# Optimization experiments

Hardware: AMD Instinct MI355X
Metric: run time of the kernel (lower is better)

The kernel has to match this reference:

```python
import jax, jax.numpy as jnp
import numpy as np

B, T, C, H = 2, 2048, 1024, 16
HD = C // H  # 64

def setup_inputs() -> dict:
    key = jax.random.key(0)
    ks = jax.random.split(key, 9)
    s = 0.02
    return {
        "x": jax.random.normal(ks[0], (B, T, C), jnp.float32),
        "Wq": jax.random.normal(ks[1], (C, C), jnp.float32) * s,
        "bq": jax.random.normal(ks[2], (C,), jnp.float32) * s,
        "Wk": jax.random.normal(ks[3], (C, C), jnp.float32) * s,
        "bk": jax.random.normal(ks[4], (C,), jnp.float32) * s,
        "Wv": jax.random.normal(ks[5], (C, C), jnp.float32) * s,
        "bv": jax.random.normal(ks[6], (C,), jnp.float32) * s,
        "Wp": jax.random.normal(ks[7], (C, C), jnp.float32) * s,
        "bp": jax.random.normal(ks[8], (C,), jnp.float32) * s,
    }

def reference(x, Wq, bq, Wk, bk, Wv, bv, Wp, bp):
    Bb, Tt, Cc = x.shape
    hd = Cc // H
    # project and split heads: [B, H, T, hd]
    def heads(W, b):
        return (x @ W.T + b).reshape(Bb, Tt, H, hd).transpose(0, 2, 1, 3)
    q, k, v = heads(Wq, bq), heads(Wk, bk), heads(Wv, bv)
    scale = 1.0 / np.sqrt(hd).astype(np.float32)
    att = jnp.einsum('bhqd,bhkd->bhqk', q, k) * scale
    causal = jnp.tril(jnp.ones((Tt, Tt), bool))
    att = jnp.where(causal[None, None], att, -jnp.inf)
    att = jax.nn.softmax(att, axis=-1)
    y = jnp.einsum('bhqk,bhkd->bhqd', att, v)
    y = y.transpose(0, 2, 1, 3).reshape(Bb, Tt, Cc)
    return y @ Wp.T + bp
```

## Files before the change

### kernel.cpp

```cpp
#include <hip/hip_runtime.h>
#include <hip/hip_bf16.h>

#define Tsz 2048
#define Csz 1024
#define Hn 16

typedef short s8v __attribute__((ext_vector_type(8)));
typedef short s4v __attribute__((ext_vector_type(4)));
typedef float f4v __attribute__((ext_vector_type(4)));

#define QSCALE (0.125f * 1.44269504088896f)

__device__ __forceinline__ short bf_bits(float x) {
    __hip_bfloat16 t = __float2bfloat16(x);
    return *reinterpret_cast<short*>(&t);
}

__device__ __forceinline__ void gload_lds(const void* g, void* l) {
    __builtin_amdgcn_global_load_lds(
        (const __attribute__((address_space(1))) void*)g,
        (__attribute__((address_space(3))) void*)l, 16, 0, 0);
}

__global__ void cvt5(const float* __restrict__ x, const float* __restrict__ wq,
                     const float* __restrict__ wk, const float* __restrict__ wv,
                     const float* __restrict__ wp,
                     short* __restrict__ xo, short* __restrict__ qo,
                     short* __restrict__ ko, short* __restrict__ vo,
                     short* __restrict__ po) {
    const int y = blockIdx.y;
    const float* in; short* out; int n;
    switch (y) {
        case 0: in = x;  out = xo; n = 2 * Tsz * Csz; break;
        case 1: in = wq; out = qo; n = Csz * Csz; break;
        case 2: in = wk; out = ko; n = Csz * Csz; break;
        case 3: in = wv; out = vo; n = Csz * Csz; break;
        default: in = wp; out = po; n = Csz * Csz; break;
    }
    int i = (blockIdx.x * blockDim.x + threadIdx.x) * 4;
    if (i >= n) return;
    float4 v = *(const float4*)(in + i);
    short4 o;
    o.x = bf_bits(v.x); o.y = bf_bits(v.y); o.z = bf_bits(v.z); o.w = bf_bits(v.w);
    *(short4*)(out + i) = o;
}

__global__ __launch_bounds__(256, 2) void qkv_gemm(
    const short* __restrict__ X,
    const short* __restrict__ Wq, const short* __restrict__ Wk, const short* __restrict__ Wv,
    const float* __restrict__ bq, const float* __restrict__ bk, const float* __restrict__ bv,
    short* __restrict__ Qo, short* __restrict__ Ko, short* __restrict__ Vto)
{
    const int z = blockIdx.z;
    const short* W = (z == 0) ? Wq : (z == 1) ? Wk : Wv;
    const float* bias = (z == 0) ? bq : (z == 1) ? bk : bv;

    __shared__ __align__(16) short Ash[128 * 32];
    __shared__ __align__(16) short Bsh[128 * 32];

    const int tid = threadIdx.x, lane = tid & 63, wave = tid >> 6;
    const int ln = lane & 15, hi = lane >> 4;
    const int m0 = blockIdx.x * 128, n0 = blockIdx.y * 128;
    const int wm = (wave >> 1) * 64, wn = (wave & 1) * 64;

    const short* Ag = X + (size_t)(m0 + (tid >> 2)) * Csz + (tid & 3) * 8;
    const short* Bg = W + (size_t)(n0 + (tid >> 2)) * Csz + (tid & 3) * 8;

    f4v acc[4][4];
    #pragma unroll
    for (int mt = 0; mt < 4; mt++)
        #pragma unroll
        for (int nt = 0; nt < 4; nt++)
            #pragma unroll
            for (int i = 0; i < 4; i++) acc[mt][nt][i] = 0.f;

    for (int k0 = 0; k0 < Csz; k0 += 32) {
        __syncthreads();
        gload_lds(Ag + k0, Ash + tid * 8);
        gload_lds(Ag + k0 + (size_t)64 * Csz, Ash + 2048 + tid * 8);
        gload_lds(Bg + k0, Bsh + tid * 8);
        gload_lds(Bg + k0 + (size_t)64 * Csz, Bsh + 2048 + tid * 8);
        __syncthreads();

        s8v af[4], bfr[4];
        #pragma unroll
        for (int mt = 0; mt < 4; mt++)
            af[mt] = *(const s8v*)(Ash + (wm + mt * 16 + ln) * 32 + hi * 8);
        #pragma unroll
        for (int nt = 0; nt < 4; nt++)
            bfr[nt] = *(const s8v*)(Bsh + (wn + nt * 16 + ln) * 32 + hi * 8);
        #pragma unroll
        for (int mt = 0; mt < 4; mt++)
            #pragma unroll
            for (int nt = 0; nt < 4; nt++)
                acc[mt][nt] = __builtin_amdgcn_mfma_f32_16x16x32_bf16(af[mt], bfr[nt], acc[mt][nt], 0, 0, 0);
    }

    const float scale = (z == 0) ? QSCALE : 1.0f;
    short* out = (z == 0) ? Qo : Ko;

    #pragma unroll
    for (int nt = 0; nt < 4; nt++) {
        const int col = n0 + wn + nt * 16 + ln;
        const float bvv = bias[col];
        #pragma unroll
        for (int mt = 0; mt < 4; mt++) {
            const int row0 = m0 + wm + mt * 16 + hi * 4;
            if (z == 2) {
                const int b = row0 >> 11, t = row0 & 2047;
                s4v pk;
                #pragma unroll
                for (int i = 0; i < 4; i++) pk[i] = bf_bits(acc[mt][nt][i] + bvv);
                *(s4v*)(Vto + (size_t)(b * 1024 + col) * Tsz + t) = pk;
            } else {
                #pragma unroll
                for (int i = 0; i < 4; i++)
                    out[(size_t)(row0 + i) * Csz + col] = bf_bits((acc[mt][nt][i] + bvv) * scale);
            }
        }
    }
}

__global__ __launch_bounds__(256, 2) void proj_gemm(
    const short* __restrict__ A, const short* __restrict__ W,
    const float* __restrict__ bias, float* __restrict__ out)
{
    __shared__ __align__(16) short Ash[128 * 32];
    __shared__ __align__(16) short Bsh[128 * 32];

    const int tid = threadIdx.x, lane = tid & 63, wave = tid >> 6;
    const int ln = lane & 15, hi = lane >> 4;
    const int m0 = blockIdx.x * 128, n0 = blockIdx.y * 128;
    const int wm = (wave >> 1) * 64, wn = (wave & 1) * 64;

    const short* Ag = A + (size_t)(m0 + (tid >> 2)) * Csz + (tid & 3) * 8;
    const short* Bg = W + (size_t)(n0 + (tid >> 2)) * Csz + (tid & 3) * 8;

    f4v acc[4][4];
    #pragma unroll
    for (int mt = 0; mt < 4; mt++)
        #pragma unroll
        for (int nt = 0; nt < 4; nt++)
            #pragma unroll
            for (int i = 0; i < 4; i++) acc[mt][nt][i] = 0.f;

    for (int k0 = 0; k0 < Csz; k0 += 32) {
        __syncthreads();
        gload_lds(Ag + k0, Ash + tid * 8);
        gload_lds(Ag + k0 + (size_t)64 * Csz, Ash + 2048 + tid * 8);
        gload_lds(Bg + k0, Bsh + tid * 8);
        gload_lds(Bg + k0 + (size_t)64 * Csz, Bsh + 2048 + tid * 8);
        __syncthreads();

        s8v af[4], bfr[4];
        #pragma unroll
        for (int mt = 0; mt < 4; mt++)
            af[mt] = *(const s8v*)(Ash + (wm + mt * 16 + ln) * 32 + hi * 8);
        #pragma unroll
        for (int nt = 0; nt < 4; nt++)
            bfr[nt] = *(const s8v*)(Bsh + (wn + nt * 16 + ln) * 32 + hi * 8);
        #pragma unroll
        for (int mt = 0; mt < 4; mt++)
            #pragma unroll
            for (int nt = 0; nt < 4; nt++)
                acc[mt][nt] = __builtin_amdgcn_mfma_f32_16x16x32_bf16(af[mt], bfr[nt], acc[mt][nt], 0, 0, 0);
    }

    #pragma unroll
    for (int nt = 0; nt < 4; nt++) {
        const int col = n0 + wn + nt * 16 + ln;
        const float bvv = bias[col];
        #pragma unroll
        for (int mt = 0; mt < 4; mt++)
            #pragma unroll
            for (int i = 0; i < 4; i++)
                out[(size_t)(m0 + wm + mt * 16 + hi * 4 + i) * Csz + col] = acc[mt][nt][i] + bvv;
    }
}

__global__ __launch_bounds__(256, 2) void attn4(
    const short* __restrict__ Q, const short* __restrict__ Kg,
    const short* __restrict__ Vt, short* __restrict__ Y)
{
    __shared__ __align__(16) short Ksh[64 * 72];
    __shared__ __align__(16) short Vsh[64 * 72];
    __shared__ __align__(16) short Psh[4][16 * 72];

    const int tid = threadIdx.x, lane = tid & 63, wave = tid >> 6;
    const int ln = lane & 15, hi = lane >> 4;
    const int p = blockIdx.x;
    const int qts[2] = { p, 31 - p };
    const int bh = blockIdx.y;
    const size_t base = (size_t)(bh >> 4) * Tsz * Csz + (size_t)(bh & 15) * 64;
    const size_t vtbase = (size_t)bh * 64 * Tsz;
    const int qrel = wave * 16 + ln;
    short* Pq = Psh[wave];

    s8v qf[2][2];
    #pragma unroll
    for (int t = 0; t < 2; t++)
        #pragma unroll
        for (int kk = 0; kk < 2; kk++)
            qf[t][kk] = *(const s8v*)(Q + base + (size_t)(qts[t] * 64 + qrel) * Csz + kk * 32 + hi * 8);

    f4v o[2][4], lacc[2];
    #pragma unroll
    for (int t = 0; t < 2; t++) {
        #pragma unroll
        for (int i = 0; i < 4; i++) lacc[t][i] = 0.f;
        #pragma unroll
        for (int dt = 0; dt < 4; dt++)
            #pragma unroll
            for (int i = 0; i < 4; i++) o[t][dt][i] = 0.f;
    }

    s8v ones;
    #pragma unroll
    for (int j = 0; j < 8; j++) ones[j] = (short)0x3F80;

    const int sr = tid >> 2, sc = (tid & 3) * 16;
    const short* Kp = Kg + base + (size_t)sr * Csz + sc;
    const short* Vp = Vt + vtbase + (size_t)sr * Tsz + sc;
    short* KshW = Ksh + sr * 72 + sc;
    short* VshW = Vsh + sr * 72 + sc;

    const int nkb = qts[1] + 1;
    for (int kb = 0; kb < nkb; kb++) {
        const int k0 = kb * 64;
        const s8v ka = *(const s8v*)(Kp + (size_t)k0 * Csz);
        const s8v kb2 = *(const s8v*)(Kp + (size_t)k0 * Csz + 8);
        const s8v va = *(const s8v*)(Vp + k0);
        const s8v vb2 = *(const s8v*)(Vp + k0 + 8);
        __syncthreads();
        *(s8v*)(KshW) = ka; *(s8v*)(KshW + 8) = kb2;
        *(s8v*)(VshW) = va; *(s8v*)(VshW + 8) = vb2;
        __syncthreads();

        s8v kf[2][4], vf[2][4];
        #pragma unroll
        for (int nt = 0; nt < 4; nt++)
            #pragma unroll
            for (int kk = 0; kk < 2; kk++) {
                kf[kk][nt] = *(const s8v*)(Ksh + (nt * 16 + ln) * 72 + kk * 32 + hi * 8);
                vf[kk][nt] = *(const s8v*)(Vsh + (nt * 16 + ln) * 72 + kk * 32 + hi * 8);
            }

        #pragma unroll
        for (int t = 0; t < 2; t++) {
            if (t == 0 && kb > qts[0]) continue;
            const bool dg = (kb == qts[t]);

            f4v s[4];
            #pragma unroll
            for (int nt = 0; nt < 4; nt++) {
                #pragma unroll
                for (int i = 0; i < 4; i++) s[nt][i] = 0.f;
                s[nt] = __builtin_amdgcn_mfma_f32_16x16x32_bf16(kf[0][nt], qf[t][0], s[nt], 0, 0, 0);
                s[nt] = __builtin_amdgcn_mfma_f32_16x16x32_bf16(kf[1][nt], qf[t][1], s[nt], 0, 0, 0);
            }

            #pragma unroll
            for (int nt = 0; nt < 4; nt++) {
                float pv[4];
                #pragma unroll
                for (int i = 0; i < 4; i++) pv[i] = exp2f(s[nt][i]);
                if (dg) {
                    const int kr = nt * 16 + hi * 4;
                    #pragma unroll
                    for (int i = 0; i < 4; i++)
                        if (kr + i > qrel) pv[i] = 0.f;
                }
                s4v w;
                #pragma unroll
                for (int i = 0; i < 4; i++) w[i] = bf_bits(pv[i]);
                *(s4v*)(Pq + ln * 72 + nt * 16 + hi * 4) = w;
            }
            const s8v pb0 = *(const s8v*)(Pq + ln * 72 + hi * 8);
            const s8v pb1 = *(const s8v*)(Pq + ln * 72 + 32 + hi * 8);

            #pragma unroll
            for (int dt = 0; dt < 4; dt++) {
                o[t][dt] = __builtin_amdgcn_mfma_f32_16x16x32_bf16(vf[0][dt], pb0, o[t][dt], 0, 0, 0);
                o[t][dt] = __builtin_amdgcn_mfma_f32_16x16x32_bf16(vf[1][dt], pb1, o[t][dt], 0, 0, 0);
            }
            lacc[t] = __builtin_amdgcn_mfma_f32_16x16x32_bf16(ones, pb0, lacc[t], 0, 0, 0);
            lacc[t] = __builtin_amdgcn_mfma_f32_16x16x32_bf16(ones, pb1, lacc[t], 0, 0, 0);
        }
    }

    #pragma unroll
    for (int t = 0; t < 2; t++) {
        const float inv = 1.0f / lacc[t][0];
        const int qrow = qts[t] * 64 + qrel;
        #pragma unroll
        for (int dt = 0; dt < 4; dt++) {
            s4v w;
            #pragma unroll
            for (int i = 0; i < 4; i++) w[i] = bf_bits(o[t][dt][i] * inv);
            *(s4v*)(Y + base + (size_t)qrow * Csz + dt * 16 + hi * 4) = w;
        }
    }
}

extern "C" void kernel_launch(void* const* d_in, const int* in_sizes, int n_in,
                              void* d_out, int out_size, void* d_ws, size_t ws_size,
                              hipStream_t stream) {
    const float* x  = (const float*)d_in[0];
    const float* Wq = (const float*)d_in[1];
    const float* bq = (const float*)d_in[2];
    const float* Wk = (const float*)d_in[3];
    const float* bk = (const float*)d_in[4];
    const float* Wv = (const float*)d_in[5];
    const float* bv = (const float*)d_in[6];
    const float* Wp = (const float*)d_in[7];
    const float* bp = (const float*)d_in[8];

    char* ws = (char*)d_ws;
    short* Xb  = (short*)(ws);
    short* Wqb = (short*)(ws + (8u  << 20));
    short* Wkb = (short*)(ws + (10u << 20));
    short* Wvb = (short*)(ws + (12u << 20));
    short* Wpb = (short*)(ws + (14u << 20));
    short* Qb  = (short*)(ws + (16u << 20));
    short* Kb  = (short*)(ws + (24u << 20));
    short* Vtb = (short*)(ws + (32u << 20));
    short* Yb  = (short*)(ws + (40u << 20));

    hipLaunchKernelGGL(cvt5, dim3(4096, 5), dim3(256), 0, stream,
                       x, Wq, Wk, Wv, Wp, Xb, Wqb, Wkb, Wvb, Wpb);

    hipLaunchKernelGGL(qkv_gemm, dim3(32, 8, 3), dim3(256), 0, stream,
                       Xb, Wqb, Wkb, Wvb, bq, bk, bv, Qb, Kb, Vtb);

    hipLaunchKernelGGL(attn4, dim3(16, 32), dim3(256), 0, stream, Qb, Kb, Vtb, Yb);

    hipLaunchKernelGGL(proj_gemm, dim3(32, 8), dim3(256), 0, stream, Yb, Wpb, bp, (float*)d_out);
}
```

Baseline: 190.4 us.

## Split attention to one query tile per block with K/V prefetch; shrink proj tiles

The attention kernel stops pairing query tiles p and 31-p in one block. It now launches one block per query tile, with heaviest tiles first and a higher occupancy bound. It also prefetches the next K/V block into registers while computing the current one, overlapping global loads with MFMA work. The projection GEMM moves to 128x64 tiles, doubling its block count for better CU fill, and qkv_gemm gets a higher launch-bounds occupancy hint. The trade-offs are uneven per-block work in attention and more register pressure from the higher occupancy targets.

Result: slower. 207.2 us (+8.8%).

```diff
diff --git a/kernel.cpp b/kernel.cpp
--- a/kernel.cpp
+++ b/kernel.cpp
@@ -45,7 +45,7 @@
     *(short4*)(out + i) = o;
 }
 
-__global__ __launch_bounds__(256, 2) void qkv_gemm(
+__global__ __launch_bounds__(256, 3) void qkv_gemm(
     const short* __restrict__ X,
     const short* __restrict__ Wq, const short* __restrict__ Wk, const short* __restrict__ Wv,
     const float* __restrict__ bq, const float* __restrict__ bk, const float* __restrict__ bv,
@@ -126,21 +126,21 @@
     const float* __restrict__ bias, float* __restrict__ out)
 {
     __shared__ __align__(16) short Ash[128 * 32];
-    __shared__ __align__(16) short Bsh[128 * 32];
+    __shared__ __align__(16) short Bsh[64 * 32];
 
     const int tid = threadIdx.x, lane = tid & 63, wave = tid >> 6;
     const int ln = lane & 15, hi = lane >> 4;
-    const int m0 = blockIdx.x * 128, n0 = blockIdx.y * 128;
-    const int wm = (wave >> 1) * 64, wn = (wave & 1) * 64;
+    const int m0 = blockIdx.x * 128, n0 = blockIdx.y * 64;
+    const int wm = (wave >> 1) * 64, wn = (wave & 1) * 32;
 
     const short* Ag = A + (size_t)(m0 + (tid >> 2)) * Csz + (tid & 3) * 8;
     const short* Bg = W + (size_t)(n0 + (tid >> 2)) * Csz + (tid & 3) * 8;
 
-    f4v acc[4][4];
+    f4v acc[4][2];
     #pragma unroll
     for (int mt = 0; mt < 4; mt++)
         #pragma unroll
-        for (int nt = 0; nt < 4; nt++)
+        for (int nt = 0; nt < 2; nt++)
             #pragma unroll
             for (int i = 0; i < 4; i++) acc[mt][nt][i] = 0.f;
 
@@ -149,25 +149,24 @@
         gload_lds(Ag + k0, Ash + tid * 8);
         gload_lds(Ag + k0 + (size_t)64 * Csz, Ash + 2048 + tid * 8);
         gload_lds(Bg + k0, Bsh + tid * 8);
-        gload_lds(Bg + k0 + (size_t)64 * Csz, Bsh + 2048 + tid * 8);
-        __syncthreads();
-
-        s8v af[4], bfr[4];
+        __syncthreads();
+
+        s8v af[4], bfr[2];
         #pragma unroll
         for (int mt = 0; mt < 4; mt++)
             af[mt] = *(const s8v*)(Ash + (wm + mt * 16 + ln) * 32 + hi * 8);
         #pragma unroll
-        for (int nt = 0; nt < 4; nt++)
+        for (int nt = 0; nt < 2; nt++)
             bfr[nt] = *(const s8v*)(Bsh + (wn + nt * 16 + ln) * 32 + hi * 8);
         #pragma unroll
         for (int mt = 0; mt < 4; mt++)
             #pragma unroll
-            for (int nt = 0; nt < 4; nt++)
+            for (int nt = 0; nt < 2; nt++)
                 acc[mt][nt] = __builtin_amdgcn_mfma_f32_16x16x32_bf16(af[mt], bfr[nt], acc[mt][nt], 0, 0, 0);
     }
 
     #pragma unroll
-    for (int nt = 0; nt < 4; nt++) {
+    for (int nt = 0; nt < 2; nt++) {
         const int col = n0 + wn + nt * 16 + ln;
         const float bvv = bias[col];
         #pragma unroll
@@ -178,7 +177,7 @@
     }
 }
 
-__global__ __launch_bounds__(256, 2) void attn4(
+__global__ __launch_bounds__(256, 4) void attn5(
     const short* __restrict__ Q, const short* __restrict__ Kg,
     const short* __restrict__ Vt, short* __restrict__ Y)
 {
@@ -188,31 +187,26 @@
 
     const int tid = threadIdx.x, lane = tid & 63, wave = tid >> 6;
     const int ln = lane & 15, hi = lane >> 4;
-    const int p = blockIdx.x;
-    const int qts[2] = { p, 31 - p };
+    const int qt = 31 - (int)blockIdx.x;
+    const int q0 = qt * 64;
     const int bh = blockIdx.y;
     const size_t base = (size_t)(bh >> 4) * Tsz * Csz + (size_t)(bh & 15) * 64;
     const size_t vtbase = (size_t)bh * 64 * Tsz;
     const int qrel = wave * 16 + ln;
     short* Pq = Psh[wave];
 
-    s8v qf[2][2];
-    #pragma unroll
-    for (int t = 0; t < 2; t++)
-        #pragma unroll
-        for (int kk = 0; kk < 2; kk++)
-            qf[t][kk] = *(const s8v*)(Q + base + (size_t)(qts[t] * 64 + qrel) * Csz + kk * 32 + hi * 8);
-
-    f4v o[2][4], lacc[2];
-    #pragma unroll
-    for (int t = 0; t < 2; t++) {
-        #pragma unroll
-        for (int i = 0; i < 4; i++) lacc[t][i] = 0.f;
-        #pragma unroll
-        for (int dt = 0; dt < 4; dt++)
-            #pragma unroll
-            for (int i = 0; i < 4; i++) o[t][dt][i] = 0.f;
-    }
+    s8v qf[2];
+    #pragma unroll
+    for (int kk = 0; kk < 2; kk++)
+        qf[kk] = *(const s8v*)(Q + base + (size_t)(q0 + qrel) * Csz + kk * 32 + hi * 8);
+
+    f4v o[4], lacc;
+    #pragma unroll
+    for (int i = 0; i < 4; i++) lacc[i] = 0.f;
+    #pragma unroll
+    for (int dt = 0; dt < 4; dt++)
+        #pragma unroll
+        for (int i = 0; i < 4; i++) o[dt][i] = 0.f;
 
     s8v ones;
     #pragma unroll
@@ -224,17 +218,23 @@
     short* KshW = Ksh + sr * 72 + sc;
     short* VshW = Vsh + sr * 72 + sc;
 
-    const int nkb = qts[1] + 1;
+    const int nkb = qt + 1;
+    s8v ka  = *(const s8v*)(Kp);
+    s8v kb2 = *(const s8v*)(Kp + 8);
+    s8v va  = *(const s8v*)(Vp);
+    s8v vb2 = *(const s8v*)(Vp + 8);
+
     for (int kb = 0; kb < nkb; kb++) {
-        const int k0 = kb * 64;
-        const s8v ka = *(const s8v*)(Kp + (size_t)k0 * Csz);
-        const s8v kb2 = *(const s8v*)(Kp + (size_t)k0 * Csz + 8);
-        const s8v va = *(const s8v*)(Vp + k0);
-        const s8v vb2 = *(const s8v*)(Vp + k0 + 8);
         __syncthreads();
         *(s8v*)(KshW) = ka; *(s8v*)(KshW + 8) = kb2;
         *(s8v*)(VshW) = va; *(s8v*)(VshW + 8) = vb2;
         __syncthreads();
+
+        const int knx = (kb + 1 < nkb) ? (kb + 1) * 64 : kb * 64;
+        ka  = *(const s8v*)(Kp + (size_t)knx * Csz);
+        kb2 = *(const s8v*)(Kp + (size_t)knx * Csz + 8);
+        va  = *(const s8v*)(Vp + knx);
+        vb2 = *(const s8v*)(Vp + knx + 8);
 
         s8v kf[2][4], vf[2][4];
         #pragma unroll
@@ -245,60 +245,53 @@
                 vf[kk][nt] = *(const s8v*)(Vsh + (nt * 16 + ln) * 72 + kk * 32 + hi * 8);
             }
 
-        #pragma unroll
-        for (int t = 0; t < 2; t++) {
-            if (t == 0 && kb > qts[0]) continue;
-            const bool dg = (kb == qts[t]);
-
-            f4v s[4];
-            #pragma unroll
-            for (int nt = 0; nt < 4; nt++) {
+        const bool dg = (kb == qt);
+
+        f4v s[4];
+        #pragma unroll
+        for (int nt = 0; nt < 4; nt++) {
+            #pragma unroll
+            for (int i = 0; i < 4; i++) s[nt][i] = 0.f;
+            s[nt] = __builtin_amdgcn_mfma_f32_16x16x32_bf16(kf[0][nt], qf[0], s[nt], 0, 0, 0);
+            s[nt] = __builtin_amdgcn_mfma_f32_16x16x32_bf16(kf[1][nt], qf[1], s[nt], 0, 0, 0);
+        }
+
+        #pragma unroll
+        for (int nt = 0; nt < 4; nt++) {
+            float pv[4];
+            #pragma unroll
+            for (int i = 0; i < 4; i++) pv[i] = exp2f(s[nt][i]);
+            if (dg) {
+                const int kr = nt * 16 + hi * 4;
                 #pragma unroll
-                for (int i = 0; i < 4; i++) s[nt][i] = 0.f;
-                s[nt] = __builtin_amdgcn_mfma_f32_16x16x32_bf16(kf[0][nt], qf[t][0], s[nt], 0, 0, 0);
-                s[nt] = __builtin_amdgcn_mfma_f32_16x16x32_bf16(kf[1][nt], qf[t][1], s[nt], 0, 0, 0);
+                for (int i = 0; i < 4; i++)
+                    if (kr + i > qrel) pv[i] = 0.f;
             }
-
-            #pragma unroll
-            for (int nt = 0; nt < 4; nt++) {
-                float pv[4];
-                #pragma unroll
-                for (int i = 0; i < 4; i++) pv[i] = exp2f(s[nt][i]);
-                if (dg) {
-                    const int kr = nt * 16 + hi * 4;
-                    #pragma unroll
-                    for (int i = 0; i < 4; i++)
-                        if (kr + i > qrel) pv[i] = 0.f;
-                }
-                s4v w;
-                #pragma unroll
-                for (int i = 0; i < 4; i++) w[i] = bf_bits(pv[i]);
-                *(s4v*)(Pq + ln * 72 + nt * 16 + hi * 4) = w;
-            }
-            const s8v pb0 = *(const s8v*)(Pq + ln * 72 + hi * 8);
-            const s8v pb1 = *(const s8v*)(Pq + ln * 72 + 32 + hi * 8);
-
-            #pragma unroll
-            for (int dt = 0; dt < 4; dt++) {
-                o[t][dt] = __builtin_amdgcn_mfma_f32_16x16x32_bf16(vf[0][dt], pb0, o[t][dt], 0, 0, 0);
-                o[t][dt] = __builtin_amdgcn_mfma_f32_16x16x32_bf16(vf[1][dt], pb1, o[t][dt], 0, 0, 0);
-            }
-            lacc[t] = __builtin_amdgcn_mfma_f32_16x16x32_bf16(ones, pb0, lacc[t], 0, 0, 0);
-            lacc[t] = __builtin_amdgcn_mfma_f32_16x16x32_bf16(ones, pb1, lacc[t], 0, 0, 0);
+            s4v w;
+            #pragma unroll
+            for (int i = 0; i < 4; i++) w[i] = bf_bits(pv[i]);
+            *(s4v*)(Pq + ln * 72 + nt * 16 + hi * 4) = w;
         }
-    }
-
-    #pragma unroll
-    for (int t = 0; t < 2; t++) {
-        const float inv = 1.0f / lacc[t][0];
-        const int qrow = qts[t] * 64 + qrel;
+        const s8v pb0 = *(const s8v*)(Pq + ln * 72 + hi * 8);
+        const s8v pb1 = *(const s8v*)(Pq + ln * 72 + 32 + hi * 8);
+
         #pragma unroll
         for (int dt = 0; dt < 4; dt++) {
-            s4v w;
-            #pragma unroll
-            for (int i = 0; i < 4; i++) w[i] = bf_bits(o[t][dt][i] * inv);
-            *(s4v*)(Y + base + (size_t)qrow * Csz + dt * 16 + hi * 4) = w;
+            o[dt] = __builtin_amdgcn_mfma_f32_16x16x32_bf16(vf[0][dt], pb0, o[dt], 0, 0, 0);
+            o[dt] = __builtin_amdgcn_mfma_f32_16x16x32_bf16(vf[1][dt], pb1, o[dt], 0, 0, 0);
         }
+        lacc = __builtin_amdgcn_mfma_f32_16x16x32_bf16(ones, pb0, lacc, 0, 0, 0);
+        lacc = __builtin_amdgcn_mfma_f32_16x16x32_bf16(ones, pb1, lacc, 0, 0, 0);
+    }
+
+    const float inv = 1.0f / lacc[0];
+    const int qrow = q0 + qrel;
+    #pragma unroll
+    for (int dt = 0; dt < 4; dt++) {
+        s4v w;
+        #pragma unroll
+        for (int i = 0; i < 4; i++) w[i] = bf_bits(o[dt][i] * inv);
+        *(s4v*)(Y + base + (size_t)qrow * Csz + dt * 16 + hi * 4) = w;
     }
 }
 
@@ -332,7 +325,7 @@
     hipLaunchKernelGGL(qkv_gemm, dim3(32, 8, 3), dim3(256), 0, stream,
                        Xb, Wqb, Wkb, Wvb, bq, bk, bv, Qb, Kb, Vtb);
 
-    hipLaunchKernelGGL(attn4, dim3(16, 32), dim3(256), 0, stream, Qb, Kb, Vtb, Yb);
-
-    hipLaunchKernelGGL(proj_gemm, dim3(32, 8), dim3(256), 0, stream, Yb, Wpb, bp, (float*)d_out);
-}
+    hipLaunchKernelGGL(attn5, dim3(32, 32), dim3(256), 0, stream, Qb, Kb, Vtb, Yb);
+
+    hipLaunchKernelGGL(proj_gemm, dim3(32, 16), dim3(256), 0, stream, Yb, Wpb, bp, (float*)d_out);
+}
```
